# Kernel tuning notes

Measured on AMD Instinct MI355X. Metric: run time of the kernel, lower is better.

Reference implementation:

```python
import jax, jax.numpy as jnp
import numpy as np

HIDDEN = 64
INPUT = 19


def _lstm_layer(x, Wih, Whh, bih, bhh):
    # x: [B, T, I]; Wih: [4H, I]; Whh: [4H, H]; biases: [4H]
    B, T, _ = x.shape
    H = Whh.shape[1]
    # Input contribution for all timesteps at once (big GEMM).
    zx = jnp.einsum('bti,gi->btg', x, Wih) + bih + bhh  # [B, T, 4H]

    def step(carry, z_t):
        h, c = carry
        z = z_t + h @ Whh.T  # [B, 4H]
        i, f, g, o = jnp.split(z, 4, axis=-1)  # torch gate order: i, f, g, o
        i = jax.nn.sigmoid(i)
        f = jax.nn.sigmoid(f)
        g = jnp.tanh(g)
        o = jax.nn.sigmoid(o)
        c = f * c + i * g
        h = o * jnp.tanh(c)
        return (h, c), h

    h0 = jnp.zeros((B, H), x.dtype)
    (_, _), hs = jax.lax.scan(step, (h0, h0), jnp.swapaxes(zx, 0, 1))
    return jnp.swapaxes(hs, 0, 1)  # [B, T, H]


def setup_inputs() -> dict:
    key = jax.random.key(0)
    ks = jax.random.split(key, 12)
    B, T = 4096, 168
    s = 1.0 / np.sqrt(HIDDEN)  # torch LSTM/Linear init scale
    u = lambda k, shape: jax.random.uniform(k, shape, jnp.float32, -s, s)
    return {
        'x': jax.random.normal(ks[0], (B, T, INPUT), jnp.float32),
        'Wih0': u(ks[1], (4 * HIDDEN, INPUT)),
        'Whh0': u(ks[2], (4 * HIDDEN, HIDDEN)),
        'bih0': u(ks[3], (4 * HIDDEN,)),
        'bhh0': u(ks[4], (4 * HIDDEN,)),
        'Wih1': u(ks[5], (4 * HIDDEN, HIDDEN)),
        'Whh1': u(ks[6], (4 * HIDDEN, HIDDEN)),
        'bih1': u(ks[7], (4 * HIDDEN,)),
        'bhh1': u(ks[8], (4 * HIDDEN,)),
        'Wfc': u(ks[9], (1, HIDDEN)),
        'bfc': u(ks[10], (1,)),
    }


def reference(x, Wih0, Whh0, bih0, bhh0, Wih1, Whh1, bih1, bhh1, Wfc, bfc):
    h1 = _lstm_layer(x, Wih0, Whh0, bih0, bhh0)   # [B, T, H]
    h2 = _lstm_layer(h1, Wih1, Whh1, bih1, bhh1)  # [B, T, H]
    out = h2[:, -1, :] @ Wfc.T + bfc              # [B, 1]
    return out.squeeze(-1)                        # [B]
```

## Files before the change

### kernel.cpp

```cpp
#include <hip/hip_runtime.h>
#include <math.h>

#define T_STEPS 168
#define INP     19
#define HID     64
#define ROWS    16
#define NTH     512
#define HSTH    72
#define XSTH    40

typedef _Float16 half8   __attribute__((ext_vector_type(8)));
typedef float    floatx4 __attribute__((ext_vector_type(4)));

#define KSIG  (-1.4426950408889634f)
#define KTANH ( 2.8853900817779268f)

#if defined(__has_builtin)
#  if __has_builtin(__builtin_amdgcn_exp2f)
#    define EXP2(x) __builtin_amdgcn_exp2f(x)
#  else
#    define EXP2(x) exp2f(x)
#  endif
#else
#  define EXP2(x) exp2f(x)
#endif

__global__ __launch_bounds__(NTH) __attribute__((amdgpu_waves_per_eu(2, 2)))
void lstm2_mfma7_kernel(const float* __restrict__ x,
                        const float* __restrict__ Wih0, const float* __restrict__ Whh0,
                        const float* __restrict__ bih0, const float* __restrict__ bhh0,
                        const float* __restrict__ Wih1, const float* __restrict__ Whh1,
                        const float* __restrict__ bih1, const float* __restrict__ bhh1,
                        const float* __restrict__ Wfc,  const float* __restrict__ bfc,
                        float* __restrict__ out)
{
    __shared__ __align__(16) _Float16 xf [2][ROWS][XSTH];
    __shared__ __align__(16) _Float16 h1f[2][ROWS][HSTH];
    __shared__ __align__(16) _Float16 h2f[2][ROWS][HSTH];
    __shared__ float hout[ROWS][HID];

    const int tid  = threadIdx.x;
    const int b0   = blockIdx.x * ROWS;
    const int wv   = tid >> 6;
    const int lane = tid & 63;
    const int quad = lane >> 4;
    const int l16  = lane & 15;
    const int kq   = quad * 8;
    const int lay  = wv >> 2;
    const int uq   = wv & 3;
    const int u    = uq * 16 + l16;

    half8 bfr[4][4];
    float bz[4];
#pragma unroll
    for (int gi = 0; gi < 4; ++gi) {
        const float sc = (gi == 2) ? KTANH : KSIG;
        const int gr = gi * 64 + u;
        if (lay == 0) {
            const float* wr = Wih0 + gr * INP;
#pragma unroll
            for (int e = 0; e < 8; ++e) {
                const int k = kq + e;
                bfr[gi][0][e] = (k < INP) ? (_Float16)(wr[k] * sc) : (_Float16)0.0f;
            }
            const float* hr = Whh0 + gr * HID;
#pragma unroll
            for (int e = 0; e < 8; ++e) {
                bfr[gi][1][e] = (_Float16)(hr[kq + e] * sc);
                bfr[gi][2][e] = (_Float16)(hr[32 + kq + e] * sc);
            }
            bfr[gi][3] = bfr[gi][2];
            bz[gi] = (bih0[gr] + bhh0[gr]) * sc;
        } else {
            const float* ir = Wih1 + gr * HID;
            const float* hr = Whh1 + gr * HID;
#pragma unroll
            for (int e = 0; e < 8; ++e) {
                bfr[gi][0][e] = (_Float16)(ir[kq + e] * sc);
                bfr[gi][1][e] = (_Float16)(ir[32 + kq + e] * sc);
                bfr[gi][2][e] = (_Float16)(hr[kq + e] * sc);
                bfr[gi][3][e] = (_Float16)(hr[32 + kq + e] * sc);
            }
            bz[gi] = (bih1[gr] + bhh1[gr]) * sc;
        }
    }

    float cst[4] = {0.f, 0.f, 0.f, 0.f};

    int srr = 0, sii = 0;
    const float* xsrc = nullptr;
    if (tid < ROWS * INP) {
        srr = tid / INP; sii = tid - srr * INP;
        xsrc = x + ((size_t)(b0 + srr) * T_STEPS) * INP + sii;
    }

    for (int e = tid; e < 2 * ROWS * XSTH; e += NTH) ((_Float16*)xf)[e] = (_Float16)0.f;
    for (int e = tid; e < 2 * ROWS * HSTH; e += NTH) {
        ((_Float16*)h1f)[e] = (_Float16)0.f;
        ((_Float16*)h2f)[e] = (_Float16)0.f;
    }
    __syncthreads();
    float xreg = 0.f;
    if (xsrc) {
        xf[0][srr][sii] = (_Float16)xsrc[0];
        xreg = xsrc[INP];
    }
    __syncthreads();

    for (int t = 0; t <= T_STEPS; ++t) {
        float xnew = 0.f;
        if (xsrc) {
            const int tn = (t + 2 < T_STEPS) ? (t + 2) : (T_STEPS - 1);
            xnew = xsrc[(size_t)tn * INP];
        }
        if (xsrc && (t + 1) < T_STEPS)
            xf[(t + 1) & 1][srr][sii] = (_Float16)xreg;

        const bool act = (lay == 0) ? (t < T_STEPS) : (t >= 1);
        if (act) {
            floatx4 acc[4];
#pragma unroll
            for (int gi = 0; gi < 4; ++gi)
                acc[gi] = (floatx4){bz[gi], bz[gi], bz[gi], bz[gi]};
            if (lay == 0) {
                const half8 ax = *(const half8*)&xf [t & 1][l16][kq];
                const half8 a0 = *(const half8*)&h1f[(t + 1) & 1][l16][kq];
                const half8 a1 = *(const half8*)&h1f[(t + 1) & 1][l16][32 + kq];
#pragma unroll
                for (int gi = 0; gi < 4; ++gi) {
                    acc[gi] = __builtin_amdgcn_mfma_f32_16x16x32_f16(ax, bfr[gi][0], acc[gi], 0, 0, 0);
                    acc[gi] = __builtin_amdgcn_mfma_f32_16x16x32_f16(a0, bfr[gi][1], acc[gi], 0, 0, 0);
                    acc[gi] = __builtin_amdgcn_mfma_f32_16x16x32_f16(a1, bfr[gi][2], acc[gi], 0, 0, 0);
                }
            } else {
                const half8 p0 = *(const half8*)&h1f[(t + 1) & 1][l16][kq];
                const half8 p1 = *(const half8*)&h1f[(t + 1) & 1][l16][32 + kq];
                const half8 q0 = *(const half8*)&h2f[t & 1][l16][kq];
                const half8 q1 = *(const half8*)&h2f[t & 1][l16][32 + kq];
#pragma unroll
                for (int gi = 0; gi < 4; ++gi) {
                    acc[gi] = __builtin_amdgcn_mfma_f32_16x16x32_f16(p0, bfr[gi][0], acc[gi], 0, 0, 0);
                    acc[gi] = __builtin_amdgcn_mfma_f32_16x16x32_f16(p1, bfr[gi][1], acc[gi], 0, 0, 0);
                    acc[gi] = __builtin_amdgcn_mfma_f32_16x16x32_f16(q0, bfr[gi][2], acc[gi], 0, 0, 0);
                    acc[gi] = __builtin_amdgcn_mfma_f32_16x16x32_f16(q1, bfr[gi][3], acc[gi], 0, 0, 0);
                }
            }
#pragma unroll
            for (int rg = 0; rg < 4; ++rg) {
                const float Ai = EXP2(acc[0][rg]);
                const float Af = EXP2(acc[1][rg]);
                const float Eg = EXP2(acc[2][rg]);
                const float Ao = EXP2(acc[3][rg]);
                const float t1 = 1.0f + Af;
                const float t2 = 1.0f + Ai;
                const float t3 = 1.0f + Eg;
                const float t4 = t2 * t3;
                const float num = fmaf(Eg - 1.0f, t1, cst[rg] * t4);
                const float cn  = num * __builtin_amdgcn_rcpf(t1 * t4);
                cst[rg] = cn;
                const float cc  = fminf(fmaxf(cn, -30.0f), 30.0f);
                const float Ec  = EXP2(KTANH * cc);
                const float hv  = (Ec - 1.0f) *
                    __builtin_amdgcn_rcpf((1.0f + Ao) * (Ec + 1.0f));
                const int row = quad * 4 + rg;
                if (lay == 0) {
                    h1f[t & 1][row][u] = (_Float16)hv;
                } else {
                    h2f[(t + 1) & 1][row][u] = (_Float16)hv;
                    if (t == T_STEPS) hout[row][u] = hv;
                }
            }
        }
        xreg = xnew;
        __syncthreads();
    }

    if (tid < ROWS) {
        float a = bfc[0];
        const float* hr = hout[tid];
#pragma unroll
        for (int k = 0; k < HID; ++k)
            a = fmaf(hr[k], Wfc[k], a);
        out[b0 + tid] = a;
    }
}

extern "C" void kernel_launch(void* const* d_in, const int* in_sizes, int n_in,
                              void* d_out, int out_size, void* d_ws, size_t ws_size,
                              hipStream_t stream) {
    const float* x    = (const float*)d_in[0];
    const float* Wih0 = (const float*)d_in[1];
    const float* Whh0 = (const float*)d_in[2];
    const float* bih0 = (const float*)d_in[3];
    const float* bhh0 = (const float*)d_in[4];
    const float* Wih1 = (const float*)d_in[5];
    const float* Whh1 = (const float*)d_in[6];
    const float* bih1 = (const float*)d_in[7];
    const float* bhh1 = (const float*)d_in[8];
    const float* Wfc  = (const float*)d_in[9];
    const float* bfc  = (const float*)d_in[10];
    float* out = (float*)d_out;

    const int B = in_sizes[0] / (T_STEPS * INP);
    const int grid = B / ROWS;

    lstm2_mfma7_kernel<<<dim3(grid), dim3(NTH), 0, stream>>>(
        x, Wih0, Whh0, bih0, bhh0, Wih1, Whh1, bih1, bhh1, Wfc, bfc, out);
}
```

Baseline: 234.3 us.

## Preload whole x sequence into shared memory before recurrence loop

Instead of streaming one timestep of x per iteration with register prefetch and a double-buffered shared tile, the kernel loads all 168 timesteps for the block's 16 rows into a shared array (about 129 KB as fp16) up front. Quad 3 reads from a zero buffer for the padded K columns. This removes the global loads and stores of x from the serial time loop. In exchange it adds a large upfront load phase with no overlap, and the big shared allocation limits how many blocks fit per CU, which may reduce occupancy.

```diff
diff --git a/kernel.cpp b/kernel.cpp
--- a/kernel.cpp
+++ b/kernel.cpp
@@ -7,7 +7,7 @@
 #define ROWS    16
 #define NTH     512
 #define HSTH    72
-#define XSTH    40
+#define XCOLS   24
 
 typedef _Float16 half8   __attribute__((ext_vector_type(8)));
 typedef float    floatx4 __attribute__((ext_vector_type(4)));
@@ -26,15 +26,16 @@
 #endif
 
 __global__ __launch_bounds__(NTH) __attribute__((amdgpu_waves_per_eu(2, 2)))
-void lstm2_mfma7_kernel(const float* __restrict__ x,
-                        const float* __restrict__ Wih0, const float* __restrict__ Whh0,
-                        const float* __restrict__ bih0, const float* __restrict__ bhh0,
-                        const float* __restrict__ Wih1, const float* __restrict__ Whh1,
-                        const float* __restrict__ bih1, const float* __restrict__ bhh1,
-                        const float* __restrict__ Wfc,  const float* __restrict__ bfc,
-                        float* __restrict__ out)
+void lstm2_mfma11_kernel(const float* __restrict__ x,
+                         const float* __restrict__ Wih0, const float* __restrict__ Whh0,
+                         const float* __restrict__ bih0, const float* __restrict__ bhh0,
+                         const float* __restrict__ Wih1, const float* __restrict__ Whh1,
+                         const float* __restrict__ bih1, const float* __restrict__ bhh1,
+                         const float* __restrict__ Wfc,  const float* __restrict__ bfc,
+                         float* __restrict__ out)
 {
-    __shared__ __align__(16) _Float16 xf [2][ROWS][XSTH];
+    __shared__ __align__(16) _Float16 xall[T_STEPS][ROWS][XCOLS];
+    __shared__ __align__(16) _Float16 zbuf[8];
     __shared__ __align__(16) _Float16 h1f[2][ROWS][HSTH];
     __shared__ __align__(16) _Float16 h2f[2][ROWS][HSTH];
     __shared__ float hout[ROWS][HID];
@@ -87,35 +88,30 @@
 
     float cst[4] = {0.f, 0.f, 0.f, 0.f};
 
-    int srr = 0, sii = 0;
-    const float* xsrc = nullptr;
-    if (tid < ROWS * INP) {
-        srr = tid / INP; sii = tid - srr * INP;
-        xsrc = x + ((size_t)(b0 + srr) * T_STEPS) * INP + sii;
-    }
-
-    for (int e = tid; e < 2 * ROWS * XSTH; e += NTH) ((_Float16*)xf)[e] = (_Float16)0.f;
-    for (int e = tid; e < 2 * ROWS * HSTH; e += NTH) {
-        ((_Float16*)h1f)[e] = (_Float16)0.f;
-        ((_Float16*)h2f)[e] = (_Float16)0.f;
+    {
+        int* p = (int*)xall;
+        for (int e = tid; e < (int)(sizeof(xall) / 4); e += NTH) p[e] = 0;
+        if (tid < 8) zbuf[tid] = (_Float16)0.f;
+        for (int e = tid; e < 2 * ROWS * HSTH; e += NTH) {
+            ((_Float16*)h1f)[e] = (_Float16)0.f;
+            ((_Float16*)h2f)[e] = (_Float16)0.f;
+        }
     }
     __syncthreads();
-    float xreg = 0.f;
-    if (xsrc) {
-        xf[0][srr][sii] = (_Float16)xsrc[0];
-        xreg = xsrc[INP];
+    {
+        const int XTOT = ROWS * T_STEPS * INP;
+        const float* xb = x + (size_t)b0 * T_STEPS * INP;
+        for (int e = tid; e < XTOT; e += NTH) {
+            const int row = e / (T_STEPS * INP);
+            const int rem = e - row * (T_STEPS * INP);
+            const int tt  = rem / INP;
+            const int kk  = rem - tt * INP;
+            xall[tt][row][kk] = (_Float16)xb[(size_t)row * T_STEPS * INP + (size_t)tt * INP + kk];
+        }
     }
     __syncthreads();
 
     for (int t = 0; t <= T_STEPS; ++t) {
-        float xnew = 0.f;
-        if (xsrc) {
-            const int tn = (t + 2 < T_STEPS) ? (t + 2) : (T_STEPS - 1);
-            xnew = xsrc[(size_t)tn * INP];
-        }
-        if (xsrc && (t + 1) < T_STEPS)
-            xf[(t + 1) & 1][srr][sii] = (_Float16)xreg;
-
         const bool act = (lay == 0) ? (t < T_STEPS) : (t >= 1);
         if (act) {
             floatx4 acc[4];
@@ -123,7 +119,8 @@
             for (int gi = 0; gi < 4; ++gi)
                 acc[gi] = (floatx4){bz[gi], bz[gi], bz[gi], bz[gi]};
             if (lay == 0) {
-                const half8 ax = *(const half8*)&xf [t & 1][l16][kq];
+                const _Float16* axp = (quad == 3) ? zbuf : &xall[t][l16][kq];
+                const half8 ax = *(const half8*)axp;
                 const half8 a0 = *(const half8*)&h1f[(t + 1) & 1][l16][kq];
                 const half8 a1 = *(const half8*)&h1f[(t + 1) & 1][l16][32 + kq];
 #pragma unroll
@@ -171,7 +168,6 @@
                 }
             }
         }
-        xreg = xnew;
         __syncthreads();
     }
 
@@ -204,6 +200,6 @@
     const int B = in_sizes[0] / (T_STEPS * INP);
     const int grid = B / ROWS;
 
-    lstm2_mfma7_kernel<<<dim3(grid), dim3(NTH), 0, stream>>>(
+    lstm2_mfma11_kernel<<<dim3(grid), dim3(NTH), 0, stream>>>(
         x, Wih0, Whh0, bih0, bhh0, Wih1, Whh1, bih1, bhh1, Wfc, bfc, out);
 }
```

Measured after the change: 250.4 us. +6.9%, slower.
